# Performance work log

Hardware: AMD Instinct MI355X
Metric: run time of the kernel (lower is better)

## Reference

```python
import jax, jax.numpy as jnp
import numpy as np

ANCHOR = 32
STRIDE = 1
K_INIT = 16           # self.k  -> kernel = sqrt(k) = 4
KSEL = 1              # topk selects 1 region


def unfold(x, ksize, stride):
    # x: (N, C, H, W) -> (N, C*ksize*ksize, oh*ow), torch.F.unfold layout (C outermost)
    N, C, H, W = x.shape
    oh = (H - ksize) // stride + 1
    ow = (W - ksize) // stride + 1
    ih = stride * jnp.arange(oh)[:, None] + jnp.arange(ksize)[None, :]   # (oh, k)
    iw = stride * jnp.arange(ow)[:, None] + jnp.arange(ksize)[None, :]   # (ow, k)
    p = x[:, :, ih[:, None, :, None], iw[None, :, None, :]]             # (N,C,oh,ow,k,k)
    p = p.transpose(0, 1, 4, 5, 2, 3).reshape(N, C * ksize * ksize, oh * ow)
    return p


def min_max_norm(x):
    lo = x.min(axis=-1, keepdims=True)
    hi = x.max(axis=-1, keepdims=True)
    return (x - lo) / (hi - lo + 1e-5)


def perturbed_topk(scores, noise, sigma):
    # scores: (B, d); noise: (B, ns, d)  ->  indicators (B, KSEL, d)
    d = scores.shape[-1]
    pert = scores[:, None, :] + noise * sigma                # (B, ns, d)
    _, idx = jax.lax.top_k(pert, KSEL)                       # (B, ns, K)
    idx = jnp.sort(idx, axis=-1)
    oh = jax.nn.one_hot(idx, d, dtype=scores.dtype)          # (B, ns, K, d)
    return oh.mean(axis=1)                                   # (B, K, d)


def setup_inputs() -> dict:
    key = jax.random.key(0)
    k1, k2, k3, k4 = jax.random.split(key, 4)
    b, c, t, h, w = 2, 3, 8, 448, 448
    n_key, L = 4, 196
    num_region = 121            # ((14-4)//1 + 1)**2
    num_samples = 500
    x = jax.random.normal(k1, (b, c, t, h, w), dtype=jnp.float32)
    score = jax.random.uniform(k2, (b, n_key, L), dtype=jnp.float32)
    noise = jax.random.normal(k3, (b * n_key, num_samples, num_region), dtype=jnp.float32)
    sigma = jnp.float32(0.05)
    group_id = jax.random.randint(k4, (b, t), 0, n_key)
    return {"x": x, "score": score, "noise": noise, "sigma": sigma, "group_id": group_id}


def reference(x, score, noise, sigma, group_id):
    b, c, t, h, w = x.shape
    _, n_key, L = score.shape
    A = ANCHOR
    gh, gw = h // A, w // A                         # 14, 14 == sqrt(L): no interpolate
    s = int(np.sqrt(K_INIT))                        # 4

    score2 = score.reshape(b * n_key, 1, gh, gw)

    # rearrange 'b c t h w -> (b t) c h w', then space-to-depth by anchor
    xb = x.transpose(0, 2, 1, 3, 4).reshape(b * t, c, h, w)
    xb = xb.reshape(b * t, c, gh, A, gw, A).transpose(0, 1, 3, 5, 2, 4)
    xb = xb.reshape(b * t, c * A * A, gh, gw)

    xp = unfold(xb, s, STRIDE).transpose(0, 2, 1)   # (b*t, R, c*A*A*s*s)
    sc = unfold(score2, s, STRIDE).mean(axis=1)     # (b*n_key, R)
    sc = min_max_norm(sc)
    R = sc.shape[1]

    ind = perturbed_topk(sc, noise, sigma)          # (b*n_key, 1, R)
    ind = ind.transpose(0, 2, 1).reshape(b, n_key, R, 1)

    # extend indicator to every frame via its keyframe group id
    full = ind[jnp.arange(b)[:, None], group_id]    # (b, t, R, 1)
    full = full.reshape(b * t, R)

    # bmm(indicator^T, x): weighted (soft-selected) patch per frame
    patches = jnp.einsum('br,brc->bc', full, xp)    # (b*t, c*A*A*s*s)

    p = patches.reshape(b, t, c, A, A, s, s)
    p = p.transpose(0, 2, 1, 5, 3, 6, 4).reshape(b, c, t, s * A, s * A)
    return p
```

## Files before the change

### kernel.cpp

```cpp
#include <hip/hip_runtime.h>

#define BB 2
#define CC 3
#define TT 8
#define HW 448
#define AA 32
#define GG 14
#define RR 11
#define NR 121
#define NKEY 4
#define NS 500
#define NCH 25
#define SPC 20

typedef unsigned short u16;
typedef unsigned int u32;

__device__ __forceinline__ float bf2f(u16 u) {
  union { u32 i; float f; } v; v.i = ((u32)u) << 16; return v.f;
}
__device__ __forceinline__ u16 f2bf(float f) {
  union { float f; u32 i; } v; v.f = f;
  u32 u = v.i;
  return (u16)((u + 0x7fffu + ((u >> 16) & 1u)) >> 16);
}

__device__ __forceinline__ bool sniff_is_f32(const void* scorev) {
  const u16* sh16 = (const u16*)scorev;
  bool bf_ok = true;
#pragma unroll
  for (int i = 0; i < 16; i++) {
    const u16 v = sh16[i];
    if (!(v == 0 || (v >= 0x2000 && v <= 0x3F80))) bf_ok = false;
  }
  return !bf_ok;
}

__device__ __forceinline__ float read_sigma(const void* sigmav, bool is_f32) {
  const u32 w0 = *(const u32*)sigmav;
  if (is_f32) { union { u32 i; float f; } v; v.i = w0; return v.f; }
  float sg = bf2f((u16)(w0 & 0xffffu));
  union { u32 i; float f; } v; v.i = w0;
  if (!(sg > -100.f && sg < 100.f) && (v.f > -100.f && v.f < 100.f)) sg = v.f;
  return sg;
}

__global__ __launch_bounds__(128) void hist_part(
    const void* __restrict__ scorev, void* __restrict__ noisev,
    const void* __restrict__ sigmav) {
  const int bk = blockIdx.x / NCH;
  const int ch = blockIdx.x % NCH;
  const int tid = threadIdx.x;

  __shared__ float nl[SPC * NR];
  __shared__ float srow[GG * GG];
  __shared__ float scn[NR];
  __shared__ int hist[NR];
  __shared__ float lohi[2];

  const bool is_f32 = sniff_is_f32(scorev);
  const float sg = read_sigma(sigmav, is_f32);

  const size_t chunk_elem = (size_t)(bk * NS + ch * SPC) * NR;

  if (is_f32) {
    const float* nb = (const float*)noisev + chunk_elem;
    for (int i = tid; i < SPC * NR; i += 128) nl[i] = nb[i];
    const float* sp = (const float*)scorev + bk * (GG * GG);
    for (int i = tid; i < GG * GG; i += 128) srow[i] = sp[i];
  } else {
    const u16* nb = (const u16*)noisev + chunk_elem;
    for (int i = tid; i < SPC * NR; i += 128) nl[i] = bf2f(nb[i]);
    const u16* sp = (const u16*)scorev + bk * (GG * GG);
    for (int i = tid; i < GG * GG; i += 128) srow[i] = bf2f(sp[i]);
  }
  __syncthreads();

  if (tid < NR) {
    hist[tid] = 0;
    const int oi = tid / RR, oj = tid - oi * RR;
    float ssum = 0.f;
#pragma unroll
    for (int ki = 0; ki < 4; ki++)
#pragma unroll
      for (int kj = 0; kj < 4; kj++) ssum += srow[(oi + ki) * GG + (oj + kj)];
    scn[tid] = ssum * 0.0625f;
  }
  __syncthreads();
  if (tid < 64) {
    float v1 = scn[tid];
    float v2 = (tid + 64 < NR) ? scn[tid + 64] : v1;
    float mn = fminf(v1, v2), mx = fmaxf(v1, v2);
#pragma unroll
    for (int off = 32; off > 0; off >>= 1) {
      mn = fminf(mn, __shfl_xor(mn, off, 64));
      mx = fmaxf(mx, __shfl_xor(mx, off, 64));
    }
    if (tid == 0) { lohi[0] = mn; lohi[1] = mx; }
  }
  __syncthreads();
  {
    const float lo = lohi[0];
    const float denom = lohi[1] - lo + 1e-5f;
    if (tid < NR) scn[tid] = (scn[tid] - lo) / denom;
  }
  __syncthreads();

  if (tid < SPC) {
    const float* npr = &nl[tid * NR];
    float bv = scn[0] + sg * npr[0];
    int bi = 0;
    for (int r = 1; r < NR; r++) {
      const float v = scn[r] + sg * npr[r];
      if (v > bv) { bv = v; bi = r; }
    }
    atomicAdd(&hist[bi], 1);
  }
  __syncthreads();

  if (tid < NR) {
    int* dst = (int*)((char*)noisev + chunk_elem * (is_f32 ? 4 : 2));
    dst[tid] = hist[tid];
  }
}

__global__ __launch_bounds__(64) void gather_kernel(
    const void* __restrict__ xv, const void* __restrict__ scorev,
    const void* __restrict__ noisev, const int* __restrict__ group_id,
    void* __restrict__ outv) {
  int blk = blockIdx.x;
  const int a1 = blk & (AA - 1); blk >>= 5;
  const int t = blk % TT; blk /= TT;
  const int c = blk % CC; const int b = blk / CC;
  const int tid = threadIdx.x;

  __shared__ __align__(16) float xs[GG][HW];
  __shared__ float ws[NR];

  const bool is_f32 = sniff_is_f32(scorev);

  if (is_f32) {
    const float* xb = (const float*)xv + ((size_t)((b * CC + c) * TT + t)) * (HW * HW);
    for (int i = tid; i < GG * (HW / 4); i += 64) {
      const int g = i / (HW / 4);
      const int c4 = i - g * (HW / 4);
      *(float4*)(&xs[g][c4 * 4]) =
          *(const float4*)(xb + (size_t)(a1 + AA * g) * HW + c4 * 4);
    }
  } else {
    const u16* xb = (const u16*)xv + ((size_t)((b * CC + c) * TT + t)) * (HW * HW);
    for (int i = tid; i < GG * (HW / 8); i += 64) {
      const int g = i / (HW / 8);
      const int c8 = i - g * (HW / 8);
      const uint4 v = *(const uint4*)(xb + (size_t)(a1 + AA * g) * HW + c8 * 8);
      float* d = &xs[g][c8 * 8];
      d[0] = bf2f((u16)(v.x & 0xffffu)); d[1] = bf2f((u16)(v.x >> 16));
      d[2] = bf2f((u16)(v.y & 0xffffu)); d[3] = bf2f((u16)(v.y >> 16));
      d[4] = bf2f((u16)(v.z & 0xffffu)); d[5] = bf2f((u16)(v.z >> 16));
      d[6] = bf2f((u16)(v.w & 0xffffu)); d[7] = bf2f((u16)(v.w >> 16));
    }
  }

  {
    const int mybk = b * NKEY + group_id[b * TT + t];
    const int esz = is_f32 ? 4 : 2;
    for (int r = tid; r < NR; r += 64) {
      int acc = 0;
#pragma unroll
      for (int ch = 0; ch < NCH; ch++) {
        const size_t chunk_elem = (size_t)(mybk * NS + ch * SPC) * NR;
        acc += *(const int*)((const char*)noisev + chunk_elem * esz + r * 4);
      }
      ws[r] = (float)acc * (1.0f / NS);
    }
  }
  __syncthreads();

  const int j4 = (tid & 31) * 4;
  const int kh = tid >> 5;
  float acc[2][4] = {{0.f, 0.f, 0.f, 0.f}, {0.f, 0.f, 0.f, 0.f}};

  for (int g = 0; g < GG; g++) {
    const float* xrow = &xs[g][j4];
#pragma unroll
    for (int oj = 0; oj < RR; oj++) {
      const float4 v = *(const float4*)(xrow + AA * oj);
#pragma unroll
      for (int q = 0; q < 2; q++) {
        const unsigned uoi = (unsigned)(g - (kh + 2 * q));
        const int idx = (uoi < RR) ? (int)(uoi * RR + oj) : 0;
        float wv = ws[idx];
        wv = (uoi < RR) ? wv : 0.0f;
        acc[q][0] += wv * v.x;
        acc[q][1] += wv * v.y;
        acc[q][2] += wv * v.z;
        acc[q][3] += wv * v.w;
      }
    }
  }

#pragma unroll
  for (int q = 0; q < 2; q++) {
    const int ki = kh + 2 * q;
    const size_t obase =
        ((size_t)((b * CC + c) * TT + t) * 128 + (ki * AA + a1)) * 128 + j4;
    if (is_f32) {
      float4 st;
      st.x = acc[q][0]; st.y = acc[q][1]; st.z = acc[q][2]; st.w = acc[q][3];
      *(float4*)((float*)outv + obase) = st;
    } else {
      uint2 ov;
      ov.x = (u32)f2bf(acc[q][0]) | ((u32)f2bf(acc[q][1]) << 16);
      ov.y = (u32)f2bf(acc[q][2]) | ((u32)f2bf(acc[q][3]) << 16);
      *(uint2*)((u16*)outv + obase) = ov;
    }
  }
}

extern "C" void kernel_launch(void* const* d_in, const int* in_sizes, int n_in,
                              void* d_out, int out_size, void* d_ws, size_t ws_size,
                              hipStream_t stream) {
  const void* x = d_in[0];
  const void* score = d_in[1];
  void* noise = d_in[2];
  const void* sigma = d_in[3];
  const int* group_id = (const int*)d_in[4];
  (void)d_ws; (void)ws_size; (void)in_sizes; (void)n_in; (void)out_size;

  hist_part<<<dim3(BB * NKEY * NCH), 128, 0, stream>>>(score, noise, sigma);
  gather_kernel<<<dim3(BB * CC * TT * AA), 64, 0, stream>>>(x, score, noise,
                                                            group_id, d_out);
}
```

Baseline: 104.2 us.

## Double gather block size and split oj across lane groups with shuffle reduce

The gather kernel now uses 128 threads per block instead of 64. Each thread accumulates all four kernel-row outputs for one column slice over a subset of horizontal region offsets. Partial sums are combined with cross-lane shuffles, and one lane group writes the result. The aim is faster staging of the shared-memory tile and more waves in flight. In exchange it adds shuffle reduction overhead and leaves some lanes idle because 11 offsets split unevenly over 4 groups.

```diff
diff --git a/kernel.cpp b/kernel.cpp
--- a/kernel.cpp
+++ b/kernel.cpp
@@ -124,7 +124,7 @@
   }
 }
 
-__global__ __launch_bounds__(64) void gather_kernel(
+__global__ __launch_bounds__(128) void gather_kernel(
     const void* __restrict__ xv, const void* __restrict__ scorev,
     const void* __restrict__ noisev, const int* __restrict__ group_id,
     void* __restrict__ outv) {
@@ -141,7 +141,7 @@
 
   if (is_f32) {
     const float* xb = (const float*)xv + ((size_t)((b * CC + c) * TT + t)) * (HW * HW);
-    for (int i = tid; i < GG * (HW / 4); i += 64) {
+    for (int i = tid; i < GG * (HW / 4); i += 128) {
       const int g = i / (HW / 4);
       const int c4 = i - g * (HW / 4);
       *(float4*)(&xs[g][c4 * 4]) =
@@ -149,7 +149,7 @@
     }
   } else {
     const u16* xb = (const u16*)xv + ((size_t)((b * CC + c) * TT + t)) * (HW * HW);
-    for (int i = tid; i < GG * (HW / 8); i += 64) {
+    for (int i = tid; i < GG * (HW / 8); i += 128) {
       const int g = i / (HW / 8);
       const int c8 = i - g * (HW / 8);
       const uint4 v = *(const uint4*)(xb + (size_t)(a1 + AA * g) * HW + c8 * 8);
@@ -161,58 +161,75 @@
     }
   }
 
-  {
+  if (tid < NR) {
     const int mybk = b * NKEY + group_id[b * TT + t];
     const int esz = is_f32 ? 4 : 2;
-    for (int r = tid; r < NR; r += 64) {
-      int acc = 0;
-#pragma unroll
-      for (int ch = 0; ch < NCH; ch++) {
-        const size_t chunk_elem = (size_t)(mybk * NS + ch * SPC) * NR;
-        acc += *(const int*)((const char*)noisev + chunk_elem * esz + r * 4);
+    int acc = 0;
+#pragma unroll
+    for (int ch = 0; ch < NCH; ch++) {
+      const size_t chunk_elem = (size_t)(mybk * NS + ch * SPC) * NR;
+      acc += *(const int*)((const char*)noisev + chunk_elem * esz + tid * 4);
+    }
+    ws[tid] = (float)acc * (1.0f / NS);
+  }
+  __syncthreads();
+
+  const int w = tid >> 6;
+  const int lane = tid & 63;
+  const int u = lane & 15;
+  const int v = lane >> 4;
+  const int ug = u + 16 * w;
+
+  float acc[4][4] = {{0.f,0.f,0.f,0.f},{0.f,0.f,0.f,0.f},
+                     {0.f,0.f,0.f,0.f},{0.f,0.f,0.f,0.f}};
+
+  for (int g = 0; g < GG; g++) {
+    const float* xrow = &xs[g][4 * ug];
+#pragma unroll
+    for (int ojj = 0; ojj < 3; ojj++) {
+      const int oj = v + 4 * ojj;
+      if (oj < RR) {
+        const float4 xv4 = *(const float4*)(xrow + AA * oj);
+#pragma unroll
+        for (int ki = 0; ki < 4; ki++) {
+          const unsigned uoi = (unsigned)(g - ki);
+          const int idx = (uoi < RR) ? (int)(uoi * RR + oj) : 0;
+          float wv = ws[idx];
+          wv = (uoi < RR) ? wv : 0.0f;
+          acc[ki][0] += wv * xv4.x;
+          acc[ki][1] += wv * xv4.y;
+          acc[ki][2] += wv * xv4.z;
+          acc[ki][3] += wv * xv4.w;
+        }
       }
-      ws[r] = (float)acc * (1.0f / NS);
-    }
-  }
-  __syncthreads();
-
-  const int j4 = (tid & 31) * 4;
-  const int kh = tid >> 5;
-  float acc[2][4] = {{0.f, 0.f, 0.f, 0.f}, {0.f, 0.f, 0.f, 0.f}};
-
-  for (int g = 0; g < GG; g++) {
-    const float* xrow = &xs[g][j4];
-#pragma unroll
-    for (int oj = 0; oj < RR; oj++) {
-      const float4 v = *(const float4*)(xrow + AA * oj);
-#pragma unroll
-      for (int q = 0; q < 2; q++) {
-        const unsigned uoi = (unsigned)(g - (kh + 2 * q));
-        const int idx = (uoi < RR) ? (int)(uoi * RR + oj) : 0;
-        float wv = ws[idx];
-        wv = (uoi < RR) ? wv : 0.0f;
-        acc[q][0] += wv * v.x;
-        acc[q][1] += wv * v.y;
-        acc[q][2] += wv * v.z;
-        acc[q][3] += wv * v.w;
+    }
+  }
+
+#pragma unroll
+  for (int ki = 0; ki < 4; ki++)
+#pragma unroll
+    for (int r = 0; r < 4; r++) {
+      float s = acc[ki][r];
+      s += __shfl_xor(s, 16, 64);
+      s += __shfl_xor(s, 32, 64);
+      acc[ki][r] = s;
+    }
+
+  if (v == 0) {
+    const size_t rowbase = (size_t)((b * CC + c) * TT + t) * (128 * 128);
+#pragma unroll
+    for (int ki = 0; ki < 4; ki++) {
+      const size_t obase = rowbase + (size_t)(ki * AA + a1) * 128 + 4 * ug;
+      if (is_f32) {
+        float4 st;
+        st.x = acc[ki][0]; st.y = acc[ki][1]; st.z = acc[ki][2]; st.w = acc[ki][3];
+        *(float4*)((float*)outv + obase) = st;
+      } else {
+        uint2 ov;
+        ov.x = (u32)f2bf(acc[ki][0]) | ((u32)f2bf(acc[ki][1]) << 16);
+        ov.y = (u32)f2bf(acc[ki][2]) | ((u32)f2bf(acc[ki][3]) << 16);
+        *(uint2*)((u16*)outv + obase) = ov;
       }
-    }
-  }
-
-#pragma unroll
-  for (int q = 0; q < 2; q++) {
-    const int ki = kh + 2 * q;
-    const size_t obase =
-        ((size_t)((b * CC + c) * TT + t) * 128 + (ki * AA + a1)) * 128 + j4;
-    if (is_f32) {
-      float4 st;
-      st.x = acc[q][0]; st.y = acc[q][1]; st.z = acc[q][2]; st.w = acc[q][3];
-      *(float4*)((float*)outv + obase) = st;
-    } else {
-      uint2 ov;
-      ov.x = (u32)f2bf(acc[q][0]) | ((u32)f2bf(acc[q][1]) << 16);
-      ov.y = (u32)f2bf(acc[q][2]) | ((u32)f2bf(acc[q][3]) << 16);
-      *(uint2*)((u16*)outv + obase) = ov;
     }
   }
 }
@@ -228,6 +245,6 @@
   (void)d_ws; (void)ws_size; (void)in_sizes; (void)n_in; (void)out_size;
 
   hist_part<<<dim3(BB * NKEY * NCH), 128, 0, stream>>>(score, noise, sigma);
-  gather_kernel<<<dim3(BB * CC * TT * AA), 64, 0, stream>>>(x, score, noise,
-                                                            group_id, d_out);
-}
+  gather_kernel<<<dim3(BB * CC * TT * AA), 128, 0, stream>>>(x, score, noise,
+                                                             group_id, d_out);
+}
```

Result: faster. 97.59 us (-6.3%).
